# Performance work log

Hardware: AMD Instinct MI355X
Metric: run time of the kernel (lower is better)

The kernel has to match this reference:

```python
import jax, jax.numpy as jnp
import numpy as np

B, S, D, H = 1, 2048, 768, 12
WIN = 128            # window_size
HALF = WIN // 2      # 64
WN = WIN + 1         # each position attends to [i-64, i+64] inclusive -> 129 keys
DH = D // H


def setup_inputs() -> dict:
    key = jax.random.key(0)
    ks = jax.random.split(key, 8)
    scale = 0.02
    return {
        "query": jax.random.normal(ks[0], (B, S, D), dtype=jnp.float32),
        "key":   jax.random.normal(ks[1], (B, S, D), dtype=jnp.float32),
        "value": jax.random.normal(ks[2], (B, S, D), dtype=jnp.float32),
        "Wq": jax.random.normal(ks[3], (D, D), dtype=jnp.float32) * scale,
        "bq": jnp.zeros((D,), dtype=jnp.float32),
        "Wk": jax.random.normal(ks[4], (D, D), dtype=jnp.float32) * scale,
        "bk": jnp.zeros((D,), dtype=jnp.float32),
        "Wv": jax.random.normal(ks[5], (D, D), dtype=jnp.float32) * scale,
        "bv": jnp.zeros((D,), dtype=jnp.float32),
        "Wo": jax.random.normal(ks[6], (D, D), dtype=jnp.float32) * scale,
        "bo": jnp.zeros((D,), dtype=jnp.float32),
    }


def reference(query, key, value, Wq, bq, Wk, bk, Wv, bv, Wo, bo):
    b, s, d = query.shape
    # Linear projections, split heads: [B,S,H,DH]
    q = (query @ Wq + bq).reshape(b, s, H, DH)
    k = (key   @ Wk + bk).reshape(b, s, H, DH)
    v = (value @ Wv + bv).reshape(b, s, H, DH)

    # Window gather indices: pos[i, j] = i - HALF + j, j in [0, WN)
    pos = jnp.arange(s)[:, None] + (jnp.arange(WN)[None, :] - HALF)  # [S, WN]
    valid = (pos >= 0) & (pos < s)                                   # [S, WN]
    idx = jnp.clip(pos, 0, s - 1)

    kw = k[:, idx]  # [B, S, WN, H, DH]
    vw = v[:, idx]  # [B, S, WN, H, DH]

    scores = jnp.einsum('bshd,bswhd->bhsw', q, kw) / np.sqrt(DH)     # [B,H,S,WN]
    scores = jnp.where(valid[None, None, :, :], scores, -jnp.inf)
    attn = jax.nn.softmax(scores, axis=-1)

    ctx = jnp.einsum('bhsw,bswhd->bshd', attn, vw).reshape(b, s, d)  # [B,S,D]
    return ctx @ Wo + bo
```

## Files before the change

### kernel.cpp

```cpp
#include <hip/hip_runtime.h>
#include <math.h>

#define S_LEN 2048
#define DM 768
#define NHEAD 12
#define DHEAD 64
#define WIN_N 129
#define HALF_W 64

typedef _Float16 half8 __attribute__((ext_vector_type(8)));
typedef _Float16 half4_t __attribute__((ext_vector_type(4)));
typedef float floatx4 __attribute__((ext_vector_type(4)));

typedef const __attribute__((address_space(1))) unsigned int* gas_ptr;
typedef __attribute__((address_space(3))) unsigned int* las_ptr;
__device__ __forceinline__ void gld_lds16(const void* g, void* l) {
  __builtin_amdgcn_global_load_lds((gas_ptr)g, (las_ptr)l, 16, 0, 0);
}

__global__ __launch_bounds__(256)
void cvt_act_kernel(const float* __restrict__ s0, const float* __restrict__ s1,
                    const float* __restrict__ s2, _Float16* __restrict__ d0,
                    _Float16* __restrict__ d1, _Float16* __restrict__ d2, int n4) {
  int z = blockIdx.z;
  const float* s = z == 0 ? s0 : z == 1 ? s1 : s2;
  _Float16* d = z == 0 ? d0 : z == 1 ? d1 : d2;
  int i = blockIdx.x * 256 + threadIdx.x;
  if (i >= n4) return;
  float4 v = ((const float4*)s)[i];
  half4_t h = {(_Float16)v.x, (_Float16)v.y, (_Float16)v.z, (_Float16)v.w};
  ((half4_t*)d)[i] = h;
}

__global__ __launch_bounds__(256)
void cvt_wt_kernel(const float* __restrict__ W0, const float* __restrict__ W1,
                   const float* __restrict__ W2, const float* __restrict__ W3,
                   _Float16* __restrict__ T0, _Float16* __restrict__ T1,
                   _Float16* __restrict__ T2, _Float16* __restrict__ T3) {
  __shared__ float t[64][65];
  int z = blockIdx.z;
  const float* W = z == 0 ? W0 : z == 1 ? W1 : z == 2 ? W2 : W3;
  _Float16* T = z == 0 ? T0 : z == 1 ? T1 : z == 2 ? T2 : T3;
  int n0 = blockIdx.x * 64, k0 = blockIdx.y * 64;
  int tx = threadIdx.x & 15, ty = threadIdx.x >> 4;
#pragma unroll
  for (int i = 0; i < 4; ++i) {
    int row = ty + i * 16;
    float4 v = *(const float4*)(W + (size_t)(k0 + row) * DM + n0 + tx * 4);
    t[row][tx * 4 + 0] = v.x; t[row][tx * 4 + 1] = v.y;
    t[row][tx * 4 + 2] = v.z; t[row][tx * 4 + 3] = v.w;
  }
  __syncthreads();
#pragma unroll
  for (int i = 0; i < 4; ++i) {
    int nn = ty + i * 16, kk = tx * 4;
    half4_t h = {(_Float16)t[kk + 0][nn], (_Float16)t[kk + 1][nn],
                 (_Float16)t[kk + 2][nn], (_Float16)t[kk + 3][nn]};
    *(half4_t*)(T + (size_t)(n0 + nn) * DM + k0 + kk) = h;
  }
}

#define GBM 128
#define GBN 128
#define GBK 64

__global__ __launch_bounds__(256, 2)
void gemm_f16_kernel(const _Float16* __restrict__ A0, const _Float16* __restrict__ A1,
                     const _Float16* __restrict__ A2, const _Float16* __restrict__ W0,
                     const _Float16* __restrict__ W1, const _Float16* __restrict__ W2,
                     const float* __restrict__ b0, const float* __restrict__ b1,
                     const float* __restrict__ b2, _Float16* __restrict__ H0,
                     _Float16* __restrict__ H1, _Float16* __restrict__ H2,
                     float* __restrict__ Cf, int fp32_out) {
  __shared__ __align__(16) _Float16 As[GBM * GBK];
  __shared__ __align__(16) _Float16 Bs[GBN * GBK];
  const int z = blockIdx.z;
  const _Float16* A = z == 0 ? A0 : z == 1 ? A1 : A2;
  const _Float16* Wt = z == 0 ? W0 : z == 1 ? W1 : W2;
  const float* bias = z == 0 ? b0 : z == 1 ? b1 : b2;
  _Float16* H = z == 0 ? H0 : z == 1 ? H1 : H2;

  const int tid = threadIdx.x;
  const int lane = tid & 63;
  const int w = tid >> 6;
  const int lr = lane & 15;
  const int lq = lane >> 4;
  const int m0 = blockIdx.y * GBM;
  const int n0 = blockIdx.x * GBN;
  const int wb = tid & 192;

  floatx4 acc[2][8] = {};

  for (int k0 = 0; k0 < DM; k0 += GBK) {
    __syncthreads();
#pragma unroll
    for (int i = 0; i < 4; ++i) {
      int c = i * 256 + tid;
      int m = c >> 3, j = c & 7;
      int jg = j ^ (m & 7);
      gld_lds16(A + (size_t)(m0 + m) * DM + k0 + jg * 8, &As[(i * 256 + wb) * 8]);
    }
#pragma unroll
    for (int i = 0; i < 4; ++i) {
      int c = i * 256 + tid;
      int n = c >> 3, j = c & 7;
      int jg = j ^ (n & 7);
      gld_lds16(Wt + (size_t)(n0 + n) * DM + k0 + jg * 8, &Bs[(i * 256 + wb) * 8]);
    }
    __syncthreads();

#pragma unroll
    for (int kh = 0; kh < 2; ++kh) {
      half8 af[2], bf[8];
#pragma unroll
      for (int mt = 0; mt < 2; ++mt) {
        int m = w * 32 + mt * 16 + lr;
        int j = (kh * 4 + lq) ^ (m & 7);
        af[mt] = *(const half8*)&As[m * GBK + j * 8];
      }
#pragma unroll
      for (int nt = 0; nt < 8; ++nt) {
        int n = nt * 16 + lr;
        int j = (kh * 4 + lq) ^ (n & 7);
        bf[nt] = *(const half8*)&Bs[n * GBK + j * 8];
      }
#pragma unroll
      for (int mt = 0; mt < 2; ++mt)
#pragma unroll
        for (int nt = 0; nt < 8; ++nt)
          acc[mt][nt] = __builtin_amdgcn_mfma_f32_16x16x32_f16(af[mt], bf[nt], acc[mt][nt], 0, 0, 0);
    }
  }

#pragma unroll
  for (int mt = 0; mt < 2; ++mt) {
    int row = m0 + w * 32 + mt * 16 + lq * 4;
#pragma unroll
    for (int nt = 0; nt < 8; ++nt) {
      int col = n0 + nt * 16 + lr;
      float bv = bias[col];
#pragma unroll
      for (int r = 0; r < 4; ++r) {
        float val = acc[mt][nt][r] + bv;
        if (fp32_out) Cf[(size_t)(row + r) * DM + col] = val;
        else H[(size_t)(row + r) * DM + col] = (_Float16)val;
      }
    }
  }
}

__global__ __launch_bounds__(256)
void vtrans_kernel(const _Float16* __restrict__ vh, _Float16* __restrict__ vt) {
  int s0t = blockIdx.x * 64, d0t = blockIdx.y * 64;
#pragma unroll
  for (int i = 0; i < 2; ++i) {
    int c = i * 256 + threadIdx.x;
    int r = c >> 3, cc = c & 7;
    half8 v = *(const half8*)(vh + (size_t)(s0t + r) * DM + d0t + cc * 8);
#pragma unroll
    for (int j = 0; j < 8; ++j)
      vt[(size_t)(d0t + cc * 8 + j) * S_LEN + s0t + r] = v[j];
  }
}

#define ATQ 32
#define AR 160

__global__ __launch_bounds__(256, 2)
void swattn_mfma_kernel(const _Float16* __restrict__ qh, const _Float16* __restrict__ kh,
                        const _Float16* __restrict__ vt, _Float16* __restrict__ ctx) {
  __shared__ __align__(16) _Float16 Qs[ATQ][72];
  __shared__ __align__(16) _Float16 Ks[AR][72];
  __shared__ __align__(16) _Float16 Vt[DHEAD][168];
  __shared__ float Sbuf[ATQ][161];
  __shared__ __align__(16) _Float16 Pbuf[ATQ][168];

  const int tid = threadIdx.x;
  const int lane = tid & 63, w = tid >> 6;
  const int lr = lane & 15, lq = lane >> 4;
  const int s0 = blockIdx.x * ATQ;
  const int h = blockIdx.y;

  {
    int r = tid >> 3, cc = tid & 7;
    half8 v = *(const half8*)(qh + (size_t)(s0 + r) * DM + h * DHEAD + cc * 8);
    *(half8*)(&Qs[r][cc * 8]) = v;
  }
#pragma unroll
  for (int i = 0; i < 5; ++i) {
    int c = i * 256 + tid;
    int r = c >> 3, cc = c & 7;
    int pos = s0 - HALF_W + r;
    pos = pos < 0 ? 0 : (pos > S_LEN - 1 ? S_LEN - 1 : pos);
    half8 v = *(const half8*)(kh + (size_t)pos * DM + h * DHEAD + cc * 8);
    *(half8*)(&Ks[r][cc * 8]) = v;
  }
#pragma unroll
  for (int i = 0; i < 5; ++i) {
    int c = i * 256 + tid;
    int row = c / 20, cc = c % 20;
    int cb = s0 - HALF_W + cc * 8;
    cb = cb < 0 ? 0 : (cb > S_LEN - 8 ? S_LEN - 8 : cb);
    half8 v = *(const half8*)(vt + (size_t)(h * DHEAD + row) * S_LEN + cb);
    *(half8*)(&Vt[row][cc * 8]) = v;
  }
  __syncthreads();

  {
    const int qt = w >> 1;
    const int ptb = (w & 1) * 5;
    half8 aq[2];
#pragma unroll
    for (int k2 = 0; k2 < 2; ++k2)
      aq[k2] = *(const half8*)(&Qs[qt * 16 + lr][k2 * 32 + lq * 8]);
#pragma unroll
    for (int i = 0; i < 5; ++i) {
      int pt = ptb + i;
      floatx4 acc = {};
#pragma unroll
      for (int k2 = 0; k2 < 2; ++k2) {
        half8 bk = *(const half8*)(&Ks[pt * 16 + lr][k2 * 32 + lq * 8]);
        acc = __builtin_amdgcn_mfma_f32_16x16x32_f16(aq[k2], bk, acc, 0, 0, 0);
      }
#pragma unroll
      for (int rr = 0; rr < 4; ++rr)
        Sbuf[qt * 16 + lq * 4 + rr][pt * 16 + lr] = acc[rr] * 0.125f;
    }
  }
  __syncthreads();

#pragma unroll
  for (int i = 0; i < 8; ++i) {
    int q = w * 8 + i;
    int p0 = lane, p1 = 64 + lane, p2 = 128 + lane;
    int g0 = s0 - HALF_W + p0, g1 = s0 - HALF_W + p1, g2 = s0 - HALF_W + p2;
    bool ok0 = (p0 >= q) && (g0 >= 0);
    bool ok1 = (p1 <= q + 128) && (g1 >= 0) && (g1 < S_LEN);
    bool ok2 = (lane < 32) && (p2 <= q + 128) && (g2 < S_LEN);
    float sv0 = ok0 ? Sbuf[q][p0] : -1e30f;
    float sv1 = ok1 ? Sbuf[q][p1] : -1e30f;
    float sv2 = ok2 ? Sbuf[q][p2] : -1e30f;
    float mx = fmaxf(sv0, fmaxf(sv1, sv2));
#pragma unroll
    for (int off = 32; off > 0; off >>= 1) mx = fmaxf(mx, __shfl_xor(mx, off, 64));
    float e0 = __expf(sv0 - mx), e1 = __expf(sv1 - mx), e2 = __expf(sv2 - mx);
    float sum = e0 + e1 + e2;
#pragma unroll
    for (int off = 32; off > 0; off >>= 1) sum += __shfl_xor(sum, off, 64);
    float inv = 1.f / sum;
    Pbuf[q][p0] = (_Float16)(e0 * inv);
    Pbuf[q][p1] = (_Float16)(e1 * inv);
    if (lane < 32) Pbuf[q][p2] = (_Float16)(e2 * inv);
  }
  __syncthreads();

  {
    const int qt = w >> 1;
    const int dt0 = (w & 1) * 2;
    floatx4 a0 = {}, a1 = {};
#pragma unroll
    for (int ks = 0; ks < 5; ++ks) {
      half8 ap = *(const half8*)(&Pbuf[qt * 16 + lr][ks * 32 + lq * 8]);
      half8 bv0 = *(const half8*)(&Vt[dt0 * 16 + lr][ks * 32 + lq * 8]);
      half8 bv1 = *(const half8*)(&Vt[(dt0 + 1) * 16 + lr][ks * 32 + lq * 8]);
      a0 = __builtin_amdgcn_mfma_f32_16x16x32_f16(ap, bv0, a0, 0, 0, 0);
      a1 = __builtin_amdgcn_mfma_f32_16x16x32_f16(ap, bv1, a1, 0, 0, 0);
    }
#pragma unroll
    for (int rr = 0; rr < 4; ++rr) {
      size_t row = (size_t)(s0 + qt * 16 + lq * 4 + rr) * DM + h * DHEAD;
      ctx[row + dt0 * 16 + lr] = (_Float16)a0[rr];
      ctx[row + (dt0 + 1) * 16 + lr] = (_Float16)a1[rr];
    }
  }
}

extern "C" void kernel_launch(void* const* d_in, const int* in_sizes, int n_in,
                              void* d_out, int out_size, void* d_ws, size_t ws_size,
                              hipStream_t stream) {
  const float* query = (const float*)d_in[0];
  const float* key   = (const float*)d_in[1];
  const float* value = (const float*)d_in[2];
  const float* Wq = (const float*)d_in[3];
  const float* bq = (const float*)d_in[4];
  const float* Wk = (const float*)d_in[5];
  const float* bk = (const float*)d_in[6];
  const float* Wv = (const float*)d_in[7];
  const float* bv = (const float*)d_in[8];
  const float* Wo = (const float*)d_in[9];
  const float* bo = (const float*)d_in[10];
  float* out = (float*)d_out;

  const size_t nel = (size_t)S_LEN * DM;
  const size_t wel = (size_t)DM * DM;
  _Float16* Aq = (_Float16*)d_ws;
  _Float16* Ak = Aq + nel;
  _Float16* Av = Ak + nel;
  _Float16* Wtq = Av + nel;
  _Float16* Wtk = Wtq + wel;
  _Float16* Wtv = Wtk + wel;
  _Float16* Wto = Wtv + wel;
  _Float16* qh = Wto + wel;
  _Float16* khb = qh + nel;
  _Float16* vhb = khb + nel;
  _Float16* Vtg = Ak;
  _Float16* ctxh = Aq;

  cvt_wt_kernel<<<dim3(12, 12, 4), 256, 0, stream>>>(Wq, Wk, Wv, Wo, Wtq, Wtk, Wtv, Wto);
  cvt_act_kernel<<<dim3(1536, 1, 3), 256, 0, stream>>>(query, key, value, Aq, Ak, Av, (int)(nel / 4));
  gemm_f16_kernel<<<dim3(DM / GBN, S_LEN / GBM, 3), 256, 0, stream>>>(
      Aq, Ak, Av, Wtq, Wtk, Wtv, bq, bk, bv, qh, khb, vhb, nullptr, 0);
  vtrans_kernel<<<dim3(S_LEN / 64, DM / 64), 256, 0, stream>>>(vhb, Vtg);
  swattn_mfma_kernel<<<dim3(S_LEN / ATQ, NHEAD), 256, 0, stream>>>(qh, khb, Vtg, ctxh);
  gemm_f16_kernel<<<dim3(DM / GBN, S_LEN / GBM, 1), 256, 0, stream>>>(
      ctxh, ctxh, ctxh, Wto, Wto, Wto, bo, bo, bo, nullptr, nullptr, nullptr, out, 1);
}
```

Measured before the change: 153.5 us.

## Fuse prep kernels, write V transposed from GEMM, 2x2 warp tiling, async LDS loads

The weight-transpose and activation-convert kernels are merged into one launch. The V projection GEMM now writes its output directly in transposed layout, which removes the separate vtrans kernel and its extra pass over memory. The GEMM warp tiling changes from 1x4 to 2x2 (64x64 per warp) to balance A and B fragment reuse. The attention kernel now fills Q/K/V shared tiles with global_load_lds and XOR swizzling instead of padded register copies, and its softmax masks are simplified. Risks are uncoalesced 8-byte transposed stores in the GEMM epilogue and possible LDS bank conflicts in the new swizzled layouts.

```diff
diff --git a/kernel.cpp b/kernel.cpp
--- a/kernel.cpp
+++ b/kernel.cpp
@@ -5,7 +5,6 @@
 #define DM 768
 #define NHEAD 12
 #define DHEAD 64
-#define WIN_N 129
 #define HALF_W 64
 
 typedef _Float16 half8 __attribute__((ext_vector_type(8)));
@@ -19,44 +18,45 @@
 }
 
 __global__ __launch_bounds__(256)
-void cvt_act_kernel(const float* __restrict__ s0, const float* __restrict__ s1,
-                    const float* __restrict__ s2, _Float16* __restrict__ d0,
-                    _Float16* __restrict__ d1, _Float16* __restrict__ d2, int n4) {
-  int z = blockIdx.z;
-  const float* s = z == 0 ? s0 : z == 1 ? s1 : s2;
-  _Float16* d = z == 0 ? d0 : z == 1 ? d1 : d2;
-  int i = blockIdx.x * 256 + threadIdx.x;
-  if (i >= n4) return;
-  float4 v = ((const float4*)s)[i];
-  half4_t h = {(_Float16)v.x, (_Float16)v.y, (_Float16)v.z, (_Float16)v.w};
-  ((half4_t*)d)[i] = h;
-}
-
-__global__ __launch_bounds__(256)
-void cvt_wt_kernel(const float* __restrict__ W0, const float* __restrict__ W1,
-                   const float* __restrict__ W2, const float* __restrict__ W3,
-                   _Float16* __restrict__ T0, _Float16* __restrict__ T1,
-                   _Float16* __restrict__ T2, _Float16* __restrict__ T3) {
+void prep_kernel(const float* __restrict__ Wq, const float* __restrict__ Wk,
+                 const float* __restrict__ Wv, const float* __restrict__ Wo,
+                 _Float16* __restrict__ Tq, _Float16* __restrict__ Tk,
+                 _Float16* __restrict__ Tv, _Float16* __restrict__ To,
+                 const float* __restrict__ qs, const float* __restrict__ ks,
+                 const float* __restrict__ vs, _Float16* __restrict__ Aq,
+                 _Float16* __restrict__ Ak, _Float16* __restrict__ Av) {
   __shared__ float t[64][65];
-  int z = blockIdx.z;
-  const float* W = z == 0 ? W0 : z == 1 ? W1 : z == 2 ? W2 : W3;
-  _Float16* T = z == 0 ? T0 : z == 1 ? T1 : z == 2 ? T2 : T3;
-  int n0 = blockIdx.x * 64, k0 = blockIdx.y * 64;
-  int tx = threadIdx.x & 15, ty = threadIdx.x >> 4;
-#pragma unroll
-  for (int i = 0; i < 4; ++i) {
-    int row = ty + i * 16;
-    float4 v = *(const float4*)(W + (size_t)(k0 + row) * DM + n0 + tx * 4);
-    t[row][tx * 4 + 0] = v.x; t[row][tx * 4 + 1] = v.y;
-    t[row][tx * 4 + 2] = v.z; t[row][tx * 4 + 3] = v.w;
-  }
-  __syncthreads();
-#pragma unroll
-  for (int i = 0; i < 4; ++i) {
-    int nn = ty + i * 16, kk = tx * 4;
-    half4_t h = {(_Float16)t[kk + 0][nn], (_Float16)t[kk + 1][nn],
-                 (_Float16)t[kk + 2][nn], (_Float16)t[kk + 3][nn]};
-    *(half4_t*)(T + (size_t)(n0 + nn) * DM + k0 + kk) = h;
+  int b = blockIdx.x;
+  if (b < 576) {
+    int z = b / 144, rem = b % 144;
+    const float* W = z == 0 ? Wq : z == 1 ? Wk : z == 2 ? Wv : Wo;
+    _Float16* T = z == 0 ? Tq : z == 1 ? Tk : z == 2 ? Tv : To;
+    int n0 = (rem % 12) * 64, k0 = (rem / 12) * 64;
+    int tx = threadIdx.x & 15, ty = threadIdx.x >> 4;
+#pragma unroll
+    for (int i = 0; i < 4; ++i) {
+      int row = ty + i * 16;
+      float4 v = *(const float4*)(W + (size_t)(k0 + row) * DM + n0 + tx * 4);
+      t[row][tx * 4 + 0] = v.x; t[row][tx * 4 + 1] = v.y;
+      t[row][tx * 4 + 2] = v.z; t[row][tx * 4 + 3] = v.w;
+    }
+    __syncthreads();
+#pragma unroll
+    for (int i = 0; i < 4; ++i) {
+      int nn = ty + i * 16, kk = tx * 4;
+      half4_t h = {(_Float16)t[kk + 0][nn], (_Float16)t[kk + 1][nn],
+                   (_Float16)t[kk + 2][nn], (_Float16)t[kk + 3][nn]};
+      *(half4_t*)(T + (size_t)(n0 + nn) * DM + k0 + kk) = h;
+    }
+  } else {
+    int i = b - 576;
+    int z = i / 1536;
+    const float* s = z == 0 ? qs : z == 1 ? ks : vs;
+    _Float16* d = z == 0 ? Aq : z == 1 ? Ak : Av;
+    int idx = (i % 1536) * 256 + threadIdx.x;
+    float4 v = ((const float4*)s)[idx];
+    half4_t h = {(_Float16)v.x, (_Float16)v.y, (_Float16)v.z, (_Float16)v.w};
+    ((half4_t*)d)[idx] = h;
   }
 }
 
@@ -70,7 +70,7 @@
                      const _Float16* __restrict__ W1, const _Float16* __restrict__ W2,
                      const float* __restrict__ b0, const float* __restrict__ b1,
                      const float* __restrict__ b2, _Float16* __restrict__ H0,
-                     _Float16* __restrict__ H1, _Float16* __restrict__ H2,
+                     _Float16* __restrict__ H1, _Float16* __restrict__ Vt,
                      float* __restrict__ Cf, int fp32_out) {
   __shared__ __align__(16) _Float16 As[GBM * GBK];
   __shared__ __align__(16) _Float16 Bs[GBN * GBK];
@@ -78,18 +78,18 @@
   const _Float16* A = z == 0 ? A0 : z == 1 ? A1 : A2;
   const _Float16* Wt = z == 0 ? W0 : z == 1 ? W1 : W2;
   const float* bias = z == 0 ? b0 : z == 1 ? b1 : b2;
-  _Float16* H = z == 0 ? H0 : z == 1 ? H1 : H2;
 
   const int tid = threadIdx.x;
   const int lane = tid & 63;
   const int w = tid >> 6;
   const int lr = lane & 15;
   const int lq = lane >> 4;
+  const int wm = w >> 1, wn = w & 1;
   const int m0 = blockIdx.y * GBM;
   const int n0 = blockIdx.x * GBN;
   const int wb = tid & 192;
 
-  floatx4 acc[2][8] = {};
+  floatx4 acc[4][4] = {};
 
   for (int k0 = 0; k0 < DM; k0 += GBK) {
     __syncthreads();
@@ -111,67 +111,62 @@
 
 #pragma unroll
     for (int kh = 0; kh < 2; ++kh) {
-      half8 af[2], bf[8];
-#pragma unroll
-      for (int mt = 0; mt < 2; ++mt) {
-        int m = w * 32 + mt * 16 + lr;
+      half8 af[4], bf[4];
+#pragma unroll
+      for (int mt = 0; mt < 4; ++mt) {
+        int m = wm * 64 + mt * 16 + lr;
         int j = (kh * 4 + lq) ^ (m & 7);
         af[mt] = *(const half8*)&As[m * GBK + j * 8];
       }
 #pragma unroll
-      for (int nt = 0; nt < 8; ++nt) {
-        int n = nt * 16 + lr;
+      for (int nt = 0; nt < 4; ++nt) {
+        int n = wn * 64 + nt * 16 + lr;
         int j = (kh * 4 + lq) ^ (n & 7);
         bf[nt] = *(const half8*)&Bs[n * GBK + j * 8];
       }
 #pragma unroll
-      for (int mt = 0; mt < 2; ++mt)
-#pragma unroll
-        for (int nt = 0; nt < 8; ++nt)
+      for (int mt = 0; mt < 4; ++mt)
+#pragma unroll
+        for (int nt = 0; nt < 4; ++nt)
           acc[mt][nt] = __builtin_amdgcn_mfma_f32_16x16x32_f16(af[mt], bf[nt], acc[mt][nt], 0, 0, 0);
     }
   }
 
 #pragma unroll
-  for (int mt = 0; mt < 2; ++mt) {
-    int row = m0 + w * 32 + mt * 16 + lq * 4;
-#pragma unroll
-    for (int nt = 0; nt < 8; ++nt) {
-      int col = n0 + nt * 16 + lr;
+  for (int mt = 0; mt < 4; ++mt) {
+    int row0 = m0 + wm * 64 + mt * 16 + lq * 4;
+#pragma unroll
+    for (int nt = 0; nt < 4; ++nt) {
+      int col = n0 + wn * 64 + nt * 16 + lr;
       float bv = bias[col];
-#pragma unroll
-      for (int r = 0; r < 4; ++r) {
-        float val = acc[mt][nt][r] + bv;
-        if (fp32_out) Cf[(size_t)(row + r) * DM + col] = val;
-        else H[(size_t)(row + r) * DM + col] = (_Float16)val;
+      if (fp32_out) {
+#pragma unroll
+        for (int rr = 0; rr < 4; ++rr)
+          Cf[(size_t)(row0 + rr) * DM + col] = acc[mt][nt][rr] + bv;
+      } else if (z == 2) {
+        half4_t o = {(_Float16)(acc[mt][nt][0] + bv), (_Float16)(acc[mt][nt][1] + bv),
+                     (_Float16)(acc[mt][nt][2] + bv), (_Float16)(acc[mt][nt][3] + bv)};
+        *(half4_t*)(Vt + (size_t)col * S_LEN + row0) = o;
+      } else {
+        _Float16* H = z == 0 ? H0 : H1;
+#pragma unroll
+        for (int rr = 0; rr < 4; ++rr)
+          H[(size_t)(row0 + rr) * DM + col] = (_Float16)(acc[mt][nt][rr] + bv);
       }
     }
-  }
-}
-
-__global__ __launch_bounds__(256)
-void vtrans_kernel(const _Float16* __restrict__ vh, _Float16* __restrict__ vt) {
-  int s0t = blockIdx.x * 64, d0t = blockIdx.y * 64;
-#pragma unroll
-  for (int i = 0; i < 2; ++i) {
-    int c = i * 256 + threadIdx.x;
-    int r = c >> 3, cc = c & 7;
-    half8 v = *(const half8*)(vh + (size_t)(s0t + r) * DM + d0t + cc * 8);
-#pragma unroll
-    for (int j = 0; j < 8; ++j)
-      vt[(size_t)(d0t + cc * 8 + j) * S_LEN + s0t + r] = v[j];
   }
 }
 
 #define ATQ 32
 #define AR 160
+#define VTC 24
 
 __global__ __launch_bounds__(256, 2)
 void swattn_mfma_kernel(const _Float16* __restrict__ qh, const _Float16* __restrict__ kh,
                         const _Float16* __restrict__ vt, _Float16* __restrict__ ctx) {
-  __shared__ __align__(16) _Float16 Qs[ATQ][72];
-  __shared__ __align__(16) _Float16 Ks[AR][72];
-  __shared__ __align__(16) _Float16 Vt[DHEAD][168];
+  __shared__ __align__(16) _Float16 Qs[ATQ * DHEAD];
+  __shared__ __align__(16) _Float16 Ks[AR * DHEAD];
+  __shared__ __align__(16) _Float16 Vs[DHEAD * VTC * 8];
   __shared__ float Sbuf[ATQ][161];
   __shared__ __align__(16) _Float16 Pbuf[ATQ][168];
 
@@ -180,29 +175,30 @@
   const int lr = lane & 15, lq = lane >> 4;
   const int s0 = blockIdx.x * ATQ;
   const int h = blockIdx.y;
+  const int wb = tid & 192;
 
   {
-    int r = tid >> 3, cc = tid & 7;
-    half8 v = *(const half8*)(qh + (size_t)(s0 + r) * DM + h * DHEAD + cc * 8);
-    *(half8*)(&Qs[r][cc * 8]) = v;
+    int r = tid >> 3, j = tid & 7;
+    int jg = j ^ (r & 7);
+    gld_lds16(qh + (size_t)(s0 + r) * DM + h * DHEAD + jg * 8, &Qs[wb * 8]);
   }
 #pragma unroll
   for (int i = 0; i < 5; ++i) {
     int c = i * 256 + tid;
-    int r = c >> 3, cc = c & 7;
+    int r = c >> 3, j = c & 7;
+    int jg = j ^ (r & 7);
     int pos = s0 - HALF_W + r;
     pos = pos < 0 ? 0 : (pos > S_LEN - 1 ? S_LEN - 1 : pos);
-    half8 v = *(const half8*)(kh + (size_t)pos * DM + h * DHEAD + cc * 8);
-    *(half8*)(&Ks[r][cc * 8]) = v;
-  }
-#pragma unroll
-  for (int i = 0; i < 5; ++i) {
+    gld_lds16(kh + (size_t)pos * DM + h * DHEAD + jg * 8, &Ks[(i * 256 + wb) * 8]);
+  }
+#pragma unroll
+  for (int i = 0; i < 6; ++i) {
     int c = i * 256 + tid;
-    int row = c / 20, cc = c % 20;
-    int cb = s0 - HALF_W + cc * 8;
+    int r = c / VTC, j = c % VTC;
+    int jg = j ^ (r & 7);
+    int cb = s0 - HALF_W + jg * 8;
     cb = cb < 0 ? 0 : (cb > S_LEN - 8 ? S_LEN - 8 : cb);
-    half8 v = *(const half8*)(vt + (size_t)(h * DHEAD + row) * S_LEN + cb);
-    *(half8*)(&Vt[row][cc * 8]) = v;
+    gld_lds16(vt + (size_t)(h * DHEAD + r) * S_LEN + cb, &Vs[(i * 256 + wb) * 8]);
   }
   __syncthreads();
 
@@ -211,15 +207,18 @@
     const int ptb = (w & 1) * 5;
     half8 aq[2];
 #pragma unroll
-    for (int k2 = 0; k2 < 2; ++k2)
-      aq[k2] = *(const half8*)(&Qs[qt * 16 + lr][k2 * 32 + lq * 8]);
+    for (int k2 = 0; k2 < 2; ++k2) {
+      int r = qt * 16 + lr, j = (k2 * 4 + lq) ^ (r & 7);
+      aq[k2] = *(const half8*)&Qs[r * DHEAD + j * 8];
+    }
 #pragma unroll
     for (int i = 0; i < 5; ++i) {
       int pt = ptb + i;
       floatx4 acc = {};
 #pragma unroll
       for (int k2 = 0; k2 < 2; ++k2) {
-        half8 bk = *(const half8*)(&Ks[pt * 16 + lr][k2 * 32 + lq * 8]);
+        int r = pt * 16 + lr, j = (k2 * 4 + lq) ^ (r & 7);
+        half8 bk = *(const half8*)&Ks[r * DHEAD + j * 8];
         acc = __builtin_amdgcn_mfma_f32_16x16x32_f16(aq[k2], bk, acc, 0, 0, 0);
       }
 #pragma unroll
@@ -233,10 +232,10 @@
   for (int i = 0; i < 8; ++i) {
     int q = w * 8 + i;
     int p0 = lane, p1 = 64 + lane, p2 = 128 + lane;
-    int g0 = s0 - HALF_W + p0, g1 = s0 - HALF_W + p1, g2 = s0 - HALF_W + p2;
+    int g0 = s0 - HALF_W + p0, g1 = s0 + lane, g2 = s0 + HALF_W + lane;
     bool ok0 = (p0 >= q) && (g0 >= 0);
-    bool ok1 = (p1 <= q + 128) && (g1 >= 0) && (g1 < S_LEN);
-    bool ok2 = (lane < 32) && (p2 <= q + 128) && (g2 < S_LEN);
+    bool ok1 = (g1 < S_LEN);
+    bool ok2 = (lane <= q) && (g2 < S_LEN);
     float sv0 = ok0 ? Sbuf[q][p0] : -1e30f;
     float sv1 = ok1 ? Sbuf[q][p1] : -1e30f;
     float sv2 = ok2 ? Sbuf[q][p2] : -1e30f;
@@ -260,9 +259,11 @@
     floatx4 a0 = {}, a1 = {};
 #pragma unroll
     for (int ks = 0; ks < 5; ++ks) {
-      half8 ap = *(const half8*)(&Pbuf[qt * 16 + lr][ks * 32 + lq * 8]);
-      half8 bv0 = *(const half8*)(&Vt[dt0 * 16 + lr][ks * 32 + lq * 8]);
-      half8 bv1 = *(const half8*)(&Vt[(dt0 + 1) * 16 + lr][ks * 32 + lq * 8]);
+      half8 ap = *(const half8*)&Pbuf[qt * 16 + lr][ks * 32 + lq * 8];
+      int r0 = dt0 * 16 + lr, r1 = (dt0 + 1) * 16 + lr;
+      int j0 = (ks * 4 + lq) ^ (r0 & 7), j1 = (ks * 4 + lq) ^ (r1 & 7);
+      half8 bv0 = *(const half8*)&Vs[(r0 * VTC + j0) * 8];
+      half8 bv1 = *(const half8*)&Vs[(r1 * VTC + j1) * 8];
       a0 = __builtin_amdgcn_mfma_f32_16x16x32_f16(ap, bv0, a0, 0, 0, 0);
       a1 = __builtin_amdgcn_mfma_f32_16x16x32_f16(ap, bv1, a1, 0, 0, 0);
     }
@@ -302,15 +303,13 @@
   _Float16* Wto = Wtv + wel;
   _Float16* qh = Wto + wel;
   _Float16* khb = qh + nel;
-  _Float16* vhb = khb + nel;
-  _Float16* Vtg = Ak;
+  _Float16* Vtg = khb + nel;
   _Float16* ctxh = Aq;
 
-  cvt_wt_kernel<<<dim3(12, 12, 4), 256, 0, stream>>>(Wq, Wk, Wv, Wo, Wtq, Wtk, Wtv, Wto);
-  cvt_act_kernel<<<dim3(1536, 1, 3), 256, 0, stream>>>(query, key, value, Aq, Ak, Av, (int)(nel / 4));
+  prep_kernel<<<dim3(576 + 4608), 256, 0, stream>>>(
+      Wq, Wk, Wv, Wo, Wtq, Wtk, Wtv, Wto, query, key, value, Aq, Ak, Av);
   gemm_f16_kernel<<<dim3(DM / GBN, S_LEN / GBM, 3), 256, 0, stream>>>(
-      Aq, Ak, Av, Wtq, Wtk, Wtv, bq, bk, bv, qh, khb, vhb, nullptr, 0);
-  vtrans_kernel<<<dim3(S_LEN / 64, DM / 64), 256, 0, stream>>>(vhb, Vtg);
+      Aq, Ak, Av, Wtq, Wtk, Wtv, bq, bk, bv, qh, khb, Vtg, nullptr, 0);
   swattn_mfma_kernel<<<dim3(S_LEN / ATQ, NHEAD), 256, 0, stream>>>(qh, khb, Vtg, ctxh);
   gemm_f16_kernel<<<dim3(DM / GBN, S_LEN / GBM, 1), 256, 0, stream>>>(
       ctxh, ctxh, ctxh, Wto, Wto, Wto, bo, bo, bo, nullptr, nullptr, nullptr, out, 1);
```

New measurement: 144.9 us. 5.6% less time.
